# Optimization experiments

Hardware: AMD Instinct MI355X
Metric: run time of the kernel (lower is better)

Reference implementation:

```python
import jax, jax.numpy as jnp
import numpy as np

B, F = 4096, 16384          # batch, total features
G, S = 512, 32              # n_groups, group_size (F = G*S, contiguous partition)
UNITS = 1


def setup_inputs() -> dict:
    key = jax.random.key(0)
    k_x, k_w = jax.random.split(key)
    x = jax.random.normal(k_x, (B, F), dtype=jnp.float32)
    # contiguous non-overlapping groups: group g owns columns [g*S, (g+1)*S)
    group_idx = jnp.arange(G * S, dtype=jnp.int64).reshape(G, S)
    # per-group multiplicative-factor weights (GroupConnected.w, HeNormal ~ scaled normal)
    w_group = jax.random.normal(k_w, (G, S), dtype=jnp.float32) * jnp.sqrt(2.0 / S)
    # final Dense kernel, kernel_initializer=Ones in the original
    fc_kernel = jnp.ones((G, UNITS), dtype=jnp.float32)
    return {"x": x, "group_idx": group_idx, "w_group": w_group, "fc_kernel": fc_kernel}


def reference(x, group_idx, w_group, fc_kernel):
    # GroupConnected: per-group gather + weighted sum, vectorized as one gather + einsum.
    gathered = x[:, group_idx]                      # [B, G, S]
    gc = jnp.einsum('bgs,gs->bg', gathered, w_group)  # [B, G]
    # TibGroupLasso.fc: Dense(units, no bias)
    return gc @ fc_kernel                           # [B, units]
```

## Files before the change

kernel.cpp:

```cpp
#include <hip/hip_runtime.h>

#define BB 4096
#define FF 16384
#define GG 512
#define SS 32
#define HALF (FF / 2)

typedef float v4f __attribute__((ext_vector_type(4)));

__global__ void build_v_kernel(const int* __restrict__ idx,
                               const float* __restrict__ w,
                               const float* __restrict__ fc,
                               float* __restrict__ v) {
    int i = blockIdx.x * blockDim.x + threadIdx.x;
    if (i < GG * SS) {
        v[idx[i]] = w[i] * fc[i >> 5];
    }
}

__global__ __launch_bounds__(256, 4) void gemv_kernel(const float* __restrict__ x,
                                                      const float* __restrict__ v,
                                                      float* __restrict__ part) {
    __shared__ v4f vs[HALF / 4];

    const int c  = blockIdx.x & 1;
    const int r0 = (blockIdx.x >> 1) << 2;
    const int tid = threadIdx.x;

    const v4f* __restrict__ vg = (const v4f*)(v + c * HALF);
    #pragma unroll
    for (int i = tid; i < HALF / 4; i += 256)
        vs[i] = vg[i];
    __syncthreads();

    const int wave = tid >> 6;
    const int lane = tid & 63;
    const int row  = r0 + wave;

    const v4f* __restrict__ x4 = (const v4f*)(x + (size_t)row * FF + c * HALF);

    v4f acc0 = {0.0f, 0.0f, 0.0f, 0.0f};
    v4f acc1 = {0.0f, 0.0f, 0.0f, 0.0f};
    #pragma unroll 4
    for (int i = lane; i < HALF / 4; i += 128) {
        v4f xa = __builtin_nontemporal_load(&x4[i]);
        v4f xb = __builtin_nontemporal_load(&x4[i + 64]);
        acc0 += xa * vs[i];
        acc1 += xb * vs[i + 64];
    }
    v4f acc = acc0 + acc1;
    float sum = (acc.x + acc.y) + (acc.z + acc.w);

    #pragma unroll
    for (int off = 32; off > 0; off >>= 1)
        sum += __shfl_down(sum, off, 64);

    if (lane == 0) part[c * BB + row] = sum;
}

__global__ void combine_kernel(const float* __restrict__ part,
                               float* __restrict__ out) {
    int i = blockIdx.x * blockDim.x + threadIdx.x;
    if (i < BB) out[i] = part[i] + part[BB + i];
}

extern "C" void kernel_launch(void* const* d_in, const int* in_sizes, int n_in,
                              void* d_out, int out_size, void* d_ws, size_t ws_size,
                              hipStream_t stream) {
    const float* x   = (const float*)d_in[0];
    const int*   idx = (const int*)d_in[1];
    const float* w   = (const float*)d_in[2];
    const float* fc  = (const float*)d_in[3];
    float* out = (float*)d_out;
    float* v    = (float*)d_ws;
    float* part = v + FF;

    build_v_kernel<<<(GG * SS + 255) / 256, 256, 0, stream>>>(idx, w, fc, v);
    gemv_kernel<<<2 * (BB / 4), 256, 0, stream>>>(x, v, part);
    combine_kernel<<<(BB + 255) / 256, 256, 0, stream>>>(part, out);
}
```

Before: 337.0 us.

## Drop LDS staging of v and read it from cache in GEMV

The GEMV no longer copies the 32 KB half of v into shared memory per block. Each wave now reads v directly from global memory through the cache, and the block-to-row mapping changes so one block's four waves cover two rows and both halves. The loop keeps four accumulators with four loads in flight, uses plain loads instead of nontemporal ones, and raises the launch-bounds occupancy hint. This removes the per-block LDS fill and barrier, which were heavy relative to each block's work, at the cost of relying on L1/L2 hits for v and giving up the nontemporal hint on x.

```diff
diff --git a/kernel.cpp b/kernel.cpp
--- a/kernel.cpp
+++ b/kernel.cpp
@@ -18,37 +18,32 @@
     }
 }
 
-__global__ __launch_bounds__(256, 4) void gemv_kernel(const float* __restrict__ x,
+__global__ __launch_bounds__(256, 8) void gemv_kernel(const float* __restrict__ x,
                                                       const float* __restrict__ v,
                                                       float* __restrict__ part) {
-    __shared__ v4f vs[HALF / 4];
-
-    const int c  = blockIdx.x & 1;
-    const int r0 = (blockIdx.x >> 1) << 2;
-    const int tid = threadIdx.x;
-
-    const v4f* __restrict__ vg = (const v4f*)(v + c * HALF);
-    #pragma unroll
-    for (int i = tid; i < HALF / 4; i += 256)
-        vs[i] = vg[i];
-    __syncthreads();
-
+    const int tid  = threadIdx.x;
     const int wave = tid >> 6;
     const int lane = tid & 63;
-    const int row  = r0 + wave;
+    const int h    = (blockIdx.x << 2) + wave;
+    const int row  = h >> 1;
+    const int c    = h & 1;
 
     const v4f* __restrict__ x4 = (const v4f*)(x + (size_t)row * FF + c * HALF);
+    const v4f* __restrict__ v4 = (const v4f*)(v + c * HALF);
 
-    v4f acc0 = {0.0f, 0.0f, 0.0f, 0.0f};
-    v4f acc1 = {0.0f, 0.0f, 0.0f, 0.0f};
-    #pragma unroll 4
-    for (int i = lane; i < HALF / 4; i += 128) {
-        v4f xa = __builtin_nontemporal_load(&x4[i]);
-        v4f xb = __builtin_nontemporal_load(&x4[i + 64]);
-        acc0 += xa * vs[i];
-        acc1 += xb * vs[i + 64];
+    v4f a0 = {0.f, 0.f, 0.f, 0.f}, a1 = a0, a2 = a0, a3 = a0;
+    #pragma unroll 2
+    for (int i = lane; i < HALF / 4; i += 256) {
+        v4f x0 = x4[i];
+        v4f x1 = x4[i + 64];
+        v4f x2 = x4[i + 128];
+        v4f x3 = x4[i + 192];
+        a0 += x0 * v4[i];
+        a1 += x1 * v4[i + 64];
+        a2 += x2 * v4[i + 128];
+        a3 += x3 * v4[i + 192];
     }
-    v4f acc = acc0 + acc1;
+    v4f acc = (a0 + a1) + (a2 + a3);
     float sum = (acc.x + acc.y) + (acc.z + acc.w);
 
     #pragma unroll
@@ -76,6 +71,6 @@
     float* part = v + FF;
 
     build_v_kernel<<<(GG * SS + 255) / 256, 256, 0, stream>>>(idx, w, fc, v);
-    gemv_kernel<<<2 * (BB / 4), 256, 0, stream>>>(x, v, part);
+    gemv_kernel<<<BB / 2, 256, 0, stream>>>(x, v, part);
     combine_kernel<<<(BB + 255) / 256, 256, 0, stream>>>(part, out);
 }
```

New measurement: 357.1 us. 6.0% more time.
